# Performance work log

Hardware: AMD Instinct MI355X
Metric: run time of the kernel (lower is better)

## Reference

```python
import jax, jax.numpy as jnp
import numpy as np

LC = 3  # number of multigrid levels


def injection1d(v):
    # fine -> coarse: take every other point, L -> (L+1)//2
    return v[..., ::2]


def interp1d(v):
    # coarse -> fine linear interpolation, L -> 2L-1
    B, C, N = v.shape
    out = jnp.zeros((B, C, 2 * N - 1), dtype=v.dtype)
    out = out.at[..., ::2].set(v)
    out = out.at[..., 1::2].set(0.5 * (v[..., :-1] + v[..., 1:]))
    return out


def mlp(xc, w1, c1, w2, c2, w3, c3):
    # pointwise (Conv1d kernel_size=1) MLP: [1 -> 64 -> 64 -> 1] with tanh
    h = jnp.tanh(jnp.einsum('oc,bcn->bon', w1, xc) + c1[:, None])
    h = jnp.tanh(jnp.einsum('oc,bcn->bon', w2, h) + c2[:, None])
    return jnp.einsum('oc,bcn->bon', w3, h) + c3[:, None]


def kernel_approximation(x, W1, b1, W2, b2, W3, b3):
    for _ in range(LC):
        x = injection1d(x)
    n = x.shape[-1]
    a = None
    n_ = 0
    for j in range(LC):
        band = mlp(x, W1[j], b1[j], W2[j], b2[j], W3[j], b3[j])  # (B, 1, n)
        if j == 0:
            a = band
            n_ = (n - 1) // 4
        else:
            a = a.at[..., n_:n_ + n].set(band)
            n_ = n_ * 2
        a = interp1d(a)
    return a  # (B, 1, 2N-1)


def toeplitz_mvp(a, u):
    # a: (B, 1, 2N-1) kernel values k(d), u: (B, 1, N)
    # w_i = sum_j a[N-1 + i - j] u_j  via circular FFT convolution of length 2N-1
    n = u.shape[-1]
    L = 2 * n - 1
    A = jnp.fft.rfft(a, n=L)
    U = jnp.fft.rfft(u, n=L)
    w = jnp.fft.irfft(A * U, n=L)
    return w[..., n - 1:]  # (B, 1, N)


def setup_inputs() -> dict:
    key = jax.random.key(0)
    ks = jax.random.split(key, 10)
    B, N = 1024, 8193
    u = jax.random.normal(ks[0], (B, 1, N), dtype=jnp.float32)
    # displacement coordinates in [-1, 1], length 2N-1, same for each batch row
    grid = jnp.linspace(-1.0, 1.0, 2 * N - 1, dtype=jnp.float32)
    x = jnp.broadcast_to(grid[None, None, :], (B, 1, 2 * N - 1)).astype(jnp.float32)
    # per-level MLP params, stacked over LC levels
    W1 = jax.random.normal(ks[1], (LC, 64, 1), dtype=jnp.float32) * 1.0
    b1 = jax.random.normal(ks[2], (LC, 64), dtype=jnp.float32) * 0.1
    W2 = jax.random.normal(ks[3], (LC, 64, 64), dtype=jnp.float32) * (1.0 / np.sqrt(64))
    b2 = jax.random.normal(ks[4], (LC, 64), dtype=jnp.float32) * 0.1
    W3 = jax.random.normal(ks[5], (LC, 1, 64), dtype=jnp.float32) * (1.0 / np.sqrt(64))
    b3 = jax.random.normal(ks[6], (LC, 1), dtype=jnp.float32) * 0.1
    return {"u": u, "x": x, "W1": W1, "b1": b1, "W2": W2, "b2": b2, "W3": W3, "b3": b3}


def reference(u, x, W1, b1, W2, b2, W3, b3):
    a = kernel_approximation(x, W1, b1, W2, b2, W3, b3)
    w = toeplitz_mvp(a, u)
    return w
```

## Files before the change

### kernel.cpp

```cpp
#include <hip/hip_runtime.h>

typedef unsigned short u16;
typedef unsigned int   u32;
typedef float  f32x4  __attribute__((ext_vector_type(4)));
typedef __bf16 bf16x8 __attribute__((ext_vector_type(8)));
typedef u16    u16x8  __attribute__((ext_vector_type(8)));

#define NB     1024
#define NN     8193
#define K2R    8256
#define NT     129
#define ABF_LEN 16704
#define NFRAG  1032

#define OFF_BANDS 0u
#define OFF_BUF1  24832u
#define OFF_BUF2  41472u
#define OFF_ABF   74496u
#define OFF_BFRAG 108032u
#define OFF_UREV  1175040u

__device__ __forceinline__ u16 f2bf(float f) {
  u32 u = __builtin_bit_cast(u32, f);
  return (u16)((u + 0x7FFFu + ((u >> 16) & 1u)) >> 16);
}
__device__ __forceinline__ float bf2f(u16 h) {
  u32 u = ((u32)h) << 16;
  return __builtin_bit_cast(float, u);
}

__global__ void k_bands(const float* __restrict__ x,
                        const float* __restrict__ W1, const float* __restrict__ b1,
                        const float* __restrict__ W2, const float* __restrict__ b2,
                        const float* __restrict__ W3, const float* __restrict__ b3,
                        float* __restrict__ bands) {
  const int j = blockIdx.y;
  __shared__ float w2s[4096];
  __shared__ float w1s[64], b1s[64], b2s[64], w3s[64];
  for (int i = threadIdx.x; i < 4096; i += 256) w2s[i] = W2[j * 4096 + i];
  if (threadIdx.x < 64) {
    w1s[threadIdx.x] = W1[j * 64 + threadIdx.x];
    b1s[threadIdx.x] = b1[j * 64 + threadIdx.x];
    b2s[threadIdx.x] = b2[j * 64 + threadIdx.x];
    w3s[threadIdx.x] = W3[j * 64 + threadIdx.x];
  }
  __syncthreads();
  const int k = blockIdx.x * 256 + threadIdx.x;
  if (k >= 2049) return;
  const float xc = x[8 * k];
  float h1[64];
  #pragma unroll
  for (int o = 0; o < 64; ++o) h1[o] = tanhf(w1s[o] * xc + b1s[o]);
  float outv = b3[j];
  for (int o = 0; o < 64; ++o) {
    float acc = b2s[o];
    #pragma unroll
    for (int c = 0; c < 64; ++c) acc += w2s[o * 64 + c] * h1[c];
    outv += w3s[o] * tanhf(acc);
  }
  bands[j * 2049 + k] = outv;
}

__global__ void k_lvl1(const float* __restrict__ bands, float* __restrict__ buf1) {
  const int i = blockIdx.x * 256 + threadIdx.x;
  if (i >= 4097) return;
  const float* bd0 = bands;
  const float* bd1 = bands + 2049;
  float v = (i & 1) ? 0.5f * (bd0[i >> 1] + bd0[(i >> 1) + 1]) : bd0[i >> 1];
  if (i >= 512 && i < 2561) v = bd1[i - 512];
  buf1[i] = v;
}

__global__ void k_lvl2(const float* __restrict__ bands, const float* __restrict__ buf1,
                       float* __restrict__ buf2) {
  const int i = blockIdx.x * 256 + threadIdx.x;
  if (i >= 8193) return;
  const float* bd2 = bands + 2 * 2049;
  float v = (i & 1) ? 0.5f * (buf1[i >> 1] + buf1[(i >> 1) + 1]) : buf1[i >> 1];
  if (i >= 1024 && i < 3073) v = bd2[i - 1024];
  buf2[i] = v;
}

__global__ void k_lvl3(const float* __restrict__ buf2, u16* __restrict__ abf) {
  const int i = blockIdx.x * 256 + threadIdx.x;
  if (i >= ABF_LEN) return;
  float v = 0.f;
  if (i <= 16384)
    v = (i & 1) ? 0.5f * (buf2[i >> 1] + buf2[(i >> 1) + 1]) : buf2[i >> 1];
  abf[i] = f2bf(v);
}

__global__ void k_urev(const float* __restrict__ u, u16* __restrict__ urev) {
  const long total = (long)NB * (K2R / 8);
  for (long c = (long)blockIdx.x * 256 + threadIdx.x; c < total;
       c += (long)gridDim.x * 256) {
    const int b = (int)(c / (K2R / 8));
    const int j = (int)(c % (K2R / 8)) * 8;
    u16x8 v;
    #pragma unroll
    for (int r = 0; r < 8; ++r) {
      const int jr = j + r;
      const float f = (jr <= 8192) ? u[(size_t)b * NN + 8192 - jr] : 0.f;
      v[r] = f2bf(f);
    }
    *(u16x8*)&urev[(size_t)b * K2R + j] = v;
  }
}

__global__ void k_bfrag(const u16* __restrict__ abf, u16* __restrict__ bfr) {
  const int g = blockIdx.x * 256 + threadIdx.x;
  if (g >= NFRAG * 64) return;
  const int t = g >> 6, l = g & 63;
  const int s = 16 * t + (l & 15) + ((l >> 4) << 3);
  u16x8 v;
  #pragma unroll
  for (int r = 0; r < 8; ++r) v[r] = abf[s + r];
  *(u16x8*)&bfr[(size_t)g * 8] = v;
}

__global__ void k_lastcol(const u16* __restrict__ urev, const u16* __restrict__ abf,
                          float* __restrict__ out) {
  const int b = blockIdx.x;
  const int tid = threadIdx.x;
  float s = 0.f;
  #pragma unroll
  for (int it = 0; it < 5; ++it) {
    const int c = tid + 256 * it;
    if (c < K2R / 8) {
      u16x8 uv = *(const u16x8*)&urev[(size_t)b * K2R + c * 8];
      u16x8 av = *(const u16x8*)&abf[8192 + c * 8];
      #pragma unroll
      for (int r = 0; r < 8; ++r) s += bf2f(uv[r]) * bf2f(av[r]);
    }
  }
  #pragma unroll
  for (int off = 32; off >= 1; off >>= 1) s += __shfl_xor(s, off, 64);
  __shared__ float red[4];
  if ((tid & 63) == 0) red[tid >> 6] = s;
  __syncthreads();
  if (tid == 0) out[(size_t)b * NN + 8192] = red[0] + red[1] + red[2] + red[3];
}

__device__ __forceinline__ void gload16(const void* g, void* l) {
  __builtin_amdgcn_global_load_lds((__attribute__((address_space(1))) void*)(void*)g,
                                   (__attribute__((address_space(3))) void*)l, 16, 0, 0);
}

__global__ __launch_bounds__(512, 2) void k_gemm(const u16* __restrict__ urev,
                                                 const u16* __restrict__ bfrag,
                                                 float* __restrict__ out) {
  __shared__ u16 Ab[2][8192];
  __shared__ u16 Bb[2][12288];
  const int tid  = threadIdx.x;
  const int lane = tid & 63;
  const int wid  = tid >> 6;
  const int wr   = wid >> 2;
  const int wc   = wid & 3;

  const int by = blockIdx.x & 7;
  const int bx = blockIdx.x >> 3;
  const int b0 = by * 128;
  const int i0 = bx * 256;
  const int F0 = bx * 16;

  const int ch0 = tid, ch1 = tid + 512;
  const u16* aSrc0 = urev + (size_t)(b0 + (ch0 >> 3)) * K2R + (((ch0 & 7) ^ ((ch0 >> 3) & 7)) << 3);
  const u16* aSrc1 = urev + (size_t)(b0 + (ch1 >> 3)) * K2R + (((ch1 & 7) ^ ((ch1 >> 3) & 7)) << 3);
  const u16* bSrc = bfrag + ((size_t)F0 << 9);

  f32x4 acc[4][4] = {};

  auto stage = [&](int buf, int t) {
    const int j0 = t << 6;
    gload16(aSrc0 + j0, &Ab[buf][ch0 << 3]);
    gload16(aSrc1 + j0, &Ab[buf][ch1 << 3]);
    const u16* bs = bSrc + ((size_t)(t << 2) << 9);
    #pragma unroll
    for (int r = 0; r < 3; ++r) {
      const int ch = tid + (r << 9);
      gload16(bs + (ch << 3), &Bb[buf][ch << 3]);
    }
  };

  auto compute = [&](int buf) {
    bf16x8 af[8], bfv[8];
    #pragma unroll
    for (int kk = 0; kk < 2; ++kk)
      #pragma unroll
      for (int m = 0; m < 4; ++m) {
        const int row  = (wr << 6) + (m << 4) + (lane & 15);
        const int slot = ((lane >> 4) + (kk << 2)) ^ (row & 7);
        af[(kk << 2) + m] = *reinterpret_cast<const bf16x8*>(&Ab[buf][(row << 6) + (slot << 3)]);
      }
    #pragma unroll
    for (int kk = 0; kk < 2; ++kk)
      #pragma unroll
      for (int n = 0; n < 4; ++n) {
        const int w = (wc << 2) + n + (kk << 1);
        bfv[(kk << 2) + n] = *reinterpret_cast<const bf16x8*>(&Bb[buf][(w << 9) + (lane << 3)]);
      }
    #pragma unroll
    for (int kk = 0; kk < 2; ++kk)
      #pragma unroll
      for (int m = 0; m < 4; ++m)
        #pragma unroll
        for (int n = 0; n < 4; ++n)
          acc[m][n] = __builtin_amdgcn_mfma_f32_16x16x32_bf16(
              af[(kk << 2) + m], bfv[(kk << 2) + n], acc[m][n], 0, 0, 0);
  };

  stage(0, 0);
  asm volatile("s_waitcnt vmcnt(0)" ::: "memory");
  __syncthreads();
  int cur = 0;
  #pragma unroll 1
  for (int t = 0; t < NT - 1; ++t) {
    stage(cur ^ 1, t + 1);
    compute(cur);
    asm volatile("s_waitcnt vmcnt(0)" ::: "memory");
    __syncthreads();
    cur ^= 1;
  }
  compute(cur);

  #pragma unroll
  for (int n = 0; n < 4; ++n) {
    const int col = i0 + (wc << 6) + (n << 4) + (lane & 15);
    #pragma unroll
    for (int m = 0; m < 4; ++m) {
      const int rowb = b0 + (wr << 6) + (m << 4) + ((lane >> 4) << 2);
      float* o = out + (size_t)rowb * NN + col;
      #pragma unroll
      for (int r = 0; r < 4; ++r) o[(size_t)r * NN] = acc[m][n][r];
    }
  }
}

extern "C" void kernel_launch(void* const* d_in, const int* in_sizes, int n_in,
                              void* d_out, int out_size, void* d_ws, size_t ws_size,
                              hipStream_t stream) {
  (void)in_sizes; (void)n_in; (void)out_size; (void)ws_size;
  const float* u  = (const float*)d_in[0];
  const float* x  = (const float*)d_in[1];
  const float* W1 = (const float*)d_in[2];
  const float* b1 = (const float*)d_in[3];
  const float* W2 = (const float*)d_in[4];
  const float* b2 = (const float*)d_in[5];
  const float* W3 = (const float*)d_in[6];
  const float* b3 = (const float*)d_in[7];
  float* out = (float*)d_out;
  char*  ws  = (char*)d_ws;

  float* bands = (float*)(ws + OFF_BANDS);
  float* buf1  = (float*)(ws + OFF_BUF1);
  float* buf2  = (float*)(ws + OFF_BUF2);
  u16*   abf   = (u16*)(ws + OFF_ABF);
  u16*   bfr   = (u16*)(ws + OFF_BFRAG);
  u16*   urev  = (u16*)(ws + OFF_UREV);

  k_bands<<<dim3(9, 3), 256, 0, stream>>>(x, W1, b1, W2, b2, W3, b3, bands);
  k_lvl1<<<17, 256, 0, stream>>>(bands, buf1);
  k_lvl2<<<33, 256, 0, stream>>>(bands, buf1, buf2);
  k_lvl3<<<66, 256, 0, stream>>>(buf2, abf);
  k_urev<<<2048, 256, 0, stream>>>(u, urev);
  k_bfrag<<<258, 256, 0, stream>>>(abf, bfr);
  k_lastcol<<<1024, 256, 0, stream>>>(urev, abf, out);
  k_gemm<<<256, 512, 0, stream>>>(urev, bfr, out);
}
```

Measured before the change: 219.9 us.

## Fuse interpolation kernels, reindex urev grid, and halve GEMM block tile

The three level-interpolation kernels are merged into a single 1024-thread block that keeps intermediate levels in shared memory, which removes two launches and their global round trips. The urev conversion kernel now uses a 2D grid, so the grid-stride loop and the 64-bit divides go away. The GEMM tile shrinks from 128x256 with 8 waves to 128x128 with 4 waves, doubling the block count to 512 and cutting LDS per block. The smaller tile lowers data reuse per block and increases A-operand reloads, in exchange for more blocks to spread across CUs.

```diff
diff --git a/kernel.cpp b/kernel.cpp
--- a/kernel.cpp
+++ b/kernel.cpp
@@ -14,8 +14,6 @@
 #define NFRAG  1032
 
 #define OFF_BANDS 0u
-#define OFF_BUF1  24832u
-#define OFF_BUF2  41472u
 #define OFF_ABF   74496u
 #define OFF_BFRAG 108032u
 #define OFF_UREV  1175040u
@@ -61,50 +59,47 @@
   bands[j * 2049 + k] = outv;
 }
 
-__global__ void k_lvl1(const float* __restrict__ bands, float* __restrict__ buf1) {
-  const int i = blockIdx.x * 256 + threadIdx.x;
-  if (i >= 4097) return;
+__global__ void k_interp(const float* __restrict__ bands, u16* __restrict__ abf) {
+  __shared__ float s1[4097];
+  __shared__ float s2[8193];
+  const int tid = threadIdx.x;
   const float* bd0 = bands;
   const float* bd1 = bands + 2049;
-  float v = (i & 1) ? 0.5f * (bd0[i >> 1] + bd0[(i >> 1) + 1]) : bd0[i >> 1];
-  if (i >= 512 && i < 2561) v = bd1[i - 512];
-  buf1[i] = v;
-}
-
-__global__ void k_lvl2(const float* __restrict__ bands, const float* __restrict__ buf1,
-                       float* __restrict__ buf2) {
-  const int i = blockIdx.x * 256 + threadIdx.x;
-  if (i >= 8193) return;
   const float* bd2 = bands + 2 * 2049;
-  float v = (i & 1) ? 0.5f * (buf1[i >> 1] + buf1[(i >> 1) + 1]) : buf1[i >> 1];
-  if (i >= 1024 && i < 3073) v = bd2[i - 1024];
-  buf2[i] = v;
-}
-
-__global__ void k_lvl3(const float* __restrict__ buf2, u16* __restrict__ abf) {
-  const int i = blockIdx.x * 256 + threadIdx.x;
-  if (i >= ABF_LEN) return;
-  float v = 0.f;
-  if (i <= 16384)
-    v = (i & 1) ? 0.5f * (buf2[i >> 1] + buf2[(i >> 1) + 1]) : buf2[i >> 1];
-  abf[i] = f2bf(v);
+  for (int i = tid; i < 4097; i += 1024) {
+    float v = (i & 1) ? 0.5f * (bd0[i >> 1] + bd0[(i >> 1) + 1]) : bd0[i >> 1];
+    if (i >= 512 && i < 2561) v = bd1[i - 512];
+    s1[i] = v;
+  }
+  __syncthreads();
+  for (int i = tid; i < 8193; i += 1024) {
+    float v = (i & 1) ? 0.5f * (s1[i >> 1] + s1[(i >> 1) + 1]) : s1[i >> 1];
+    if (i >= 1024 && i < 3073) v = bd2[i - 1024];
+    s2[i] = v;
+  }
+  __syncthreads();
+  for (int i = tid; i < ABF_LEN; i += 1024) {
+    float v = 0.f;
+    if (i <= 16384)
+      v = (i & 1) ? 0.5f * (s2[i >> 1] + s2[(i >> 1) + 1]) : s2[i >> 1];
+    abf[i] = f2bf(v);
+  }
 }
 
 __global__ void k_urev(const float* __restrict__ u, u16* __restrict__ urev) {
-  const long total = (long)NB * (K2R / 8);
-  for (long c = (long)blockIdx.x * 256 + threadIdx.x; c < total;
-       c += (long)gridDim.x * 256) {
-    const int b = (int)(c / (K2R / 8));
-    const int j = (int)(c % (K2R / 8)) * 8;
-    u16x8 v;
-    #pragma unroll
-    for (int r = 0; r < 8; ++r) {
-      const int jr = j + r;
-      const float f = (jr <= 8192) ? u[(size_t)b * NN + 8192 - jr] : 0.f;
-      v[r] = f2bf(f);
-    }
-    *(u16x8*)&urev[(size_t)b * K2R + j] = v;
-  }
+  const int b = blockIdx.y;
+  const int c = blockIdx.x * 256 + threadIdx.x;
+  if (c >= K2R / 8) return;
+  const int j0 = c * 8;
+  const float* ub = u + (size_t)b * NN;
+  u16x8 v;
+  #pragma unroll
+  for (int r = 0; r < 8; ++r) {
+    const int jr = j0 + r;
+    const float f = (jr <= 8192) ? ub[8192 - jr] : 0.f;
+    v[r] = f2bf(f);
+  }
+  *(u16x8*)&urev[(size_t)b * K2R + j0] = v;
 }
 
 __global__ void k_bfrag(const u16* __restrict__ abf, u16* __restrict__ bfr) {
@@ -146,38 +141,42 @@
                                    (__attribute__((address_space(3))) void*)l, 16, 0, 0);
 }
 
-__global__ __launch_bounds__(512, 2) void k_gemm(const u16* __restrict__ urev,
+__global__ __launch_bounds__(256, 2) void k_gemm(const u16* __restrict__ urev,
                                                  const u16* __restrict__ bfrag,
                                                  float* __restrict__ out) {
   __shared__ u16 Ab[2][8192];
-  __shared__ u16 Bb[2][12288];
+  __shared__ u16 Bb[2][6144];
   const int tid  = threadIdx.x;
   const int lane = tid & 63;
   const int wid  = tid >> 6;
-  const int wr   = wid >> 2;
-  const int wc   = wid & 3;
+  const int wr   = wid >> 1;
+  const int wc   = wid & 1;
 
   const int by = blockIdx.x & 7;
   const int bx = blockIdx.x >> 3;
   const int b0 = by * 128;
-  const int i0 = bx * 256;
-  const int F0 = bx * 16;
-
-  const int ch0 = tid, ch1 = tid + 512;
-  const u16* aSrc0 = urev + (size_t)(b0 + (ch0 >> 3)) * K2R + (((ch0 & 7) ^ ((ch0 >> 3) & 7)) << 3);
-  const u16* aSrc1 = urev + (size_t)(b0 + (ch1 >> 3)) * K2R + (((ch1 & 7) ^ ((ch1 >> 3) & 7)) << 3);
-  const u16* bSrc = bfrag + ((size_t)F0 << 9);
+  const int i0 = bx * 128;
+  const int F0 = bx * 8;
+
+  const u16* aSrc[4];
+  #pragma unroll
+  for (int r = 0; r < 4; ++r) {
+    const int ch = tid + (r << 8);
+    aSrc[r] = urev + (size_t)(b0 + (ch >> 3)) * K2R + (((ch & 7) ^ ((ch >> 3) & 7)) << 3);
+  }
+  const u16* bBase = bfrag + ((size_t)F0 << 9);
 
   f32x4 acc[4][4] = {};
 
   auto stage = [&](int buf, int t) {
     const int j0 = t << 6;
-    gload16(aSrc0 + j0, &Ab[buf][ch0 << 3]);
-    gload16(aSrc1 + j0, &Ab[buf][ch1 << 3]);
-    const u16* bs = bSrc + ((size_t)(t << 2) << 9);
+    #pragma unroll
+    for (int r = 0; r < 4; ++r)
+      gload16(aSrc[r] + j0, &Ab[buf][(tid + (r << 8)) << 3]);
+    const u16* bs = bBase + ((size_t)t << 11);
     #pragma unroll
     for (int r = 0; r < 3; ++r) {
-      const int ch = tid + (r << 9);
+      const int ch = tid + (r << 8);
       gload16(bs + (ch << 3), &Bb[buf][ch << 3]);
     }
   };
@@ -252,18 +251,14 @@
   char*  ws  = (char*)d_ws;
 
   float* bands = (float*)(ws + OFF_BANDS);
-  float* buf1  = (float*)(ws + OFF_BUF1);
-  float* buf2  = (float*)(ws + OFF_BUF2);
   u16*   abf   = (u16*)(ws + OFF_ABF);
   u16*   bfr   = (u16*)(ws + OFF_BFRAG);
   u16*   urev  = (u16*)(ws + OFF_UREV);
 
   k_bands<<<dim3(9, 3), 256, 0, stream>>>(x, W1, b1, W2, b2, W3, b3, bands);
-  k_lvl1<<<17, 256, 0, stream>>>(bands, buf1);
-  k_lvl2<<<33, 256, 0, stream>>>(bands, buf1, buf2);
-  k_lvl3<<<66, 256, 0, stream>>>(buf2, abf);
-  k_urev<<<2048, 256, 0, stream>>>(u, urev);
+  k_interp<<<1, 1024, 0, stream>>>(bands, abf);
+  k_urev<<<dim3(5, 1024), 256, 0, stream>>>(u, urev);
   k_bfrag<<<258, 256, 0, stream>>>(abf, bfr);
   k_lastcol<<<1024, 256, 0, stream>>>(urev, abf, out);
-  k_gemm<<<256, 512, 0, stream>>>(urev, bfr, out);
-}
+  k_gemm<<<512, 256, 0, stream>>>(urev, bfr, out);
+}
```

Result: slower. 225.3 us (+2.5%).
